# Optimization experiments

Hardware: AMD Instinct MI355X
Metric: run time of the kernel (lower is better)

The kernel has to match this reference:

```python
import jax, jax.numpy as jnp
import numpy as np

EPS = 1.1920929e-07  # torch float32 eps used by nn.RMSNorm(elementwise_affine=False)
MAX_LR = 0.01        # default_step_transform_max_lr


def rmsnorm(x):
    return x * jax.lax.rsqrt(jnp.mean(jnp.square(x), axis=-1, keepdims=True) + EPS)


def assoc_scan(gates, inputs):
    # first-order recurrence x_t = gates_t * x_{t-1} + inputs_t along axis=1
    gates = jnp.broadcast_to(gates, inputs.shape)

    def combine(a, b):
        ag, ax = a
        bg, bx = b
        return (ag * bg, bg * ax + bx)

    _, out = jax.lax.associative_scan(combine, (gates, inputs), axis=1)
    return out


def setup_inputs():
    key = jax.random.key(0)
    ks = jax.random.split(key, 12)
    b, t, dim, heads, d, c = 4, 8192, 512, 8, 64, 64
    di = heads * d
    sc_dim = dim ** -0.5
    sc_d = d ** -0.5
    return {
        'seq': jax.random.normal(ks[0], (b, t, dim), jnp.float32),
        'w1': jax.random.normal(ks[1], (d, d), jnp.float32) * sc_d,
        'w2': jax.random.normal(ks[2], (d, d), jnp.float32) * sc_d,
        'Wq': jax.random.normal(ks[3], (dim, di), jnp.float32) * sc_dim,
        'Wkv': jax.random.normal(ks[4], (dim, 2 * di), jnp.float32) * sc_dim,
        'Wstep': jax.random.normal(ks[5], (dim, heads), jnp.float32) * sc_dim,
        'Wmom': jax.random.normal(ks[6], (dim, heads), jnp.float32) * sc_dim,
        'Wdecay': jax.random.normal(ks[7], (dim, heads), jnp.float32) * sc_dim,
        'Wgate': jax.random.normal(ks[8], (dim, heads), jnp.float32) * sc_dim,
        'Wcombine': jax.random.normal(ks[9], (di, dim), jnp.float32) * (di ** -0.5),
        'gamma': jnp.zeros((heads, 1, d), jnp.float32),
        'chunk_size': 64,
    }


def _forward(seq, w1, w2, Wq, Wkv, Wstep, Wmom, Wdecay, Wgate, Wcombine, gamma, c):
    b, t, dim = seq.shape
    heads = Wstep.shape[1]
    d = w1.shape[0]
    n = t // c          # number of chunks (seq_len assumed multiple of chunk_size)
    bh = b * heads

    # ---------------- store_memories ----------------
    s = rmsnorm(seq)  # store_norm
    # adaptive per-token lr: sigmoid * max_lr, per head -> (bh, n, c)
    lr = jax.nn.sigmoid(jnp.einsum('btd,dh->bth', s, Wstep)) * MAX_LR
    lr = lr.transpose(0, 2, 1).reshape(bh, n, c)
    # per-chunk momentum / decay gates from chunk-mean of seq
    s_chunk = s.reshape(b, n, c, dim).mean(axis=2)
    mom_gate = jax.nn.sigmoid(jnp.einsum('bnd,dh->bnh', s_chunk, Wmom)).transpose(0, 2, 1).reshape(bh, n, 1)
    decay = jax.nn.sigmoid(jnp.einsum('bnd,dh->bnh', s_chunk, Wdecay)).transpose(0, 2, 1).reshape(bh, n, 1)
    # keys / values, split heads, chunked -> (bh, n, c, d)
    kv = jnp.einsum('btd,de->bte', s, Wkv)
    k, v = jnp.split(kv, 2, axis=-1)
    split = lambda x: x.reshape(b, t, heads, d).transpose(0, 2, 1, 3).reshape(bh, n, c, d)
    k, v = split(k), split(v)

    def chunk_loss(ws, kc, lrc, vc):
        x = kc @ ws[0]
        x = jax.nn.silu(x) @ ws[1]
        return jnp.sum(jnp.mean(jnp.square(x - vc), axis=-1) * lrc)

    # per-sample (per bh, per chunk) grads of the tiny MLP
    grad_fn = jax.grad(chunk_loss, argnums=0)
    g1, g2 = jax.vmap(jax.vmap(grad_fn, in_axes=(None, 0, 0, 0)), in_axes=(None, 0, 0, 0))((w1, w2), k, lr, v)

    updates = []
    for g in (g1, g2):
        flat = (-g).reshape(bh, n, d * d)        # surprises
        momentum = assoc_scan(mom_gate, flat)     # momentum recurrence
        upd = assoc_scan(1.0 - decay, momentum)   # decayed weight-update recurrence
        updates.append(upd.reshape(bh, n, d, d))

    # ---------------- retrieve_memories ----------------
    r = rmsnorm(seq)[:, c - 1:]                   # retrieve_norm + causal shift
    pad = (-r.shape[1]) % c                       # pad to multiple of chunk_size (= c-1 here)
    r = jnp.pad(r, ((0, 0), (0, pad), (0, 0)))    # (b, n*c, dim)
    q = jnp.einsum('btd,de->bte', r, Wq)
    qs = q.reshape(b, n * c, heads, d).transpose(0, 2, 1, 3).reshape(bh, n, c, d)
    # apply per-chunk fast weights (base + update)
    x = jnp.einsum('bncd,bnde->bnce', qs, w1 + updates[0])
    x = jax.nn.silu(x)
    x = jnp.einsum('bncd,bnde->bnce', x, w2 + updates[1])
    vals = x.reshape(b, heads, n * c, d)
    vals = rmsnorm(vals) * (gamma + 1.0)          # MultiheadRMSNorm (gamma zeros-init)
    gate = jax.nn.sigmoid(jnp.einsum('btd,dh->bth', r, Wgate))  # retrieve_gate
    vals = vals * gate.transpose(0, 2, 1)[..., None]
    out = vals.transpose(0, 2, 1, 3).reshape(b, n * c, heads * d)  # merge heads
    out = jnp.einsum('bte,ed->btd', out, Wcombine)                 # combine_heads
    out = jnp.pad(out, ((0, 0), (c - 1, 0), (0, 0)))[:, :t]       # shift back, crop
    return out


def reference(seq, w1, w2, Wq, Wkv, Wstep, Wmom, Wdecay, Wgate, Wcombine, gamma, chunk_size):
    return _forward(seq, w1, w2, Wq, Wkv, Wstep, Wmom, Wdecay, Wgate, Wcombine, gamma, chunk_size)
```

## Files before the change

kernel.cpp:

```cpp
#include <hip/hip_runtime.h>
#include <cstdint>

#define EPS     1.1920929e-07f
#define MAX_LR  0.01f
#define BB      4
#define TT      8192
#define DIMM    512
#define HH      8
#define DD      64
#define CC      64
#define NN      128
#define BHH     32
#define LDSP    72

typedef __attribute__((ext_vector_type(8))) short short8;
typedef __attribute__((ext_vector_type(4))) float f32x4;

__device__ __forceinline__ float sigmoidf_(float x){ return 1.0f/(1.0f+__expf(-x)); }
__device__ __forceinline__ float bf2f(uint32_t lo16){ return __uint_as_float(lo16<<16); }
__device__ __forceinline__ uint16_t f2bf(float f){
    uint32_t x = __float_as_uint(f);
    return (uint16_t)((x + 0x7fffu + ((x>>16)&1u)) >> 16);
}
__device__ __forceinline__ uint32_t pk2(float a, float b){
    return (uint32_t)f2bf(a) | ((uint32_t)f2bf(b)<<16);
}
__device__ __forceinline__ void gload_lds16(const uint16_t* g, uint16_t* l){
    __builtin_amdgcn_global_load_lds(
        (const __attribute__((address_space(1))) unsigned int*)g,
        (__attribute__((address_space(3))) unsigned int*)l, 16, 0, 0);
}

__device__ __forceinline__ void gemm64(const uint16_t* A, const uint16_t* B,
                                       int strip, int q, int col, f32x4* acc)
{
    #pragma unroll
    for (int ks=0; ks<64; ks+=32){
        short8 af = *(const short8*)&A[(strip*16+col)*LDSP + ks + q*8];
        #pragma unroll
        for (int nt=0;nt<4;nt++){
            short8 bf = *(const short8*)&B[(nt*16+col)*LDSP + ks + q*8];
            acc[nt] = __builtin_amdgcn_mfma_f32_16x16x32_bf16(af, bf, acc[nt], 0,0,0);
        }
    }
}

__device__ __forceinline__ void gemm64g(const uint16_t* __restrict__ Ag,
                                        const uint16_t* B,
                                        int strip, int q, int col, f32x4* acc)
{
    #pragma unroll
    for (int ks=0; ks<64; ks+=32){
        short8 af = *(const short8*)&Ag[(strip*16+col)*DD + ks + q*8];
        #pragma unroll
        for (int nt=0;nt<4;nt++){
            short8 bf = *(const short8*)&B[(nt*16+col)*LDSP + ks + q*8];
            acc[nt] = __builtin_amdgcn_mfma_f32_16x16x32_bf16(af, bf, acc[nt], 0,0,0);
        }
    }
}

__global__ __launch_bounds__(256) void k_prep(
    const float* __restrict__ Wkv, const float* __restrict__ Wq,
    const float* __restrict__ Wcomb, const float* __restrict__ Wstep,
    const float* __restrict__ Wgate, const float* __restrict__ w1,
    const float* __restrict__ w2,
    uint16_t* __restrict__ btkv, uint16_t* __restrict__ btq,
    uint16_t* __restrict__ btc, uint16_t* __restrict__ wsg,
    uint16_t* __restrict__ w1t_bf, uint16_t* __restrict__ w2t_bf,
    uint16_t* __restrict__ w2b_bf, float* __restrict__ w1t_f,
    float* __restrict__ w2t_f)
{
    __shared__ float tile[32][33];
    __shared__ float t1[64][65];
    __shared__ float t2[64][65];
    int blk = blockIdx.x;
    if (blk < 1024){
        const float* in; uint16_t* out; int Ncols; int i;
        if (blk < 512){ in=Wkv; out=btkv; Ncols=1024; i=blk; }
        else if (blk < 768){ in=Wq; out=btq; Ncols=512; i=blk-512; }
        else { in=Wcomb; out=btc; Ncols=512; i=blk-768; }
        int nx = Ncols>>5;
        int bx = (i % nx)*32, by = (i / nx)*32;
        int lx = threadIdx.x&31, ly = threadIdx.x>>5;
        #pragma unroll
        for (int r=0;r<4;r++)
            tile[ly+8*r][lx] = in[(size_t)(by+ly+8*r)*Ncols + bx+lx];
        __syncthreads();
        #pragma unroll
        for (int r=0;r<4;r++)
            out[(size_t)(bx+ly+8*r)*DIMM + by+lx] = f2bf(tile[lx][ly+8*r]);
    } else if (blk < 1056){
        int g = (blk-1024)*256 + threadIdx.x;
        int j = g >> 9, k = g & 511;
        float v = (j < HH) ? Wstep[k*HH + j] : Wgate[k*HH + (j-HH)];
        wsg[j*DIMM + k] = f2bf(v);
    } else {
        int tx = threadIdx.x & 63, ty = threadIdx.x >> 6;
        #pragma unroll
        for (int i=0;i<16;i++){
            int row = ty*16 + i;
            float v1 = w1[row*DD + tx];
            float v2 = w2[row*DD + tx];
            t1[row][tx] = v1;
            t2[row][tx] = v2;
            w2b_bf[row*DD + tx] = f2bf(v2);
        }
        __syncthreads();
        #pragma unroll
        for (int i=0;i<16;i++){
            int row = ty*16 + i;
            float v1 = t1[tx][row];
            float v2 = t2[tx][row];
            w1t_f[row*DD + tx] = v1;
            w1t_bf[row*DD + tx] = f2bf(v1);
            w2t_f[row*DD + tx] = v2;
            w2t_bf[row*DD + tx] = f2bf(v2);
        }
    }
}

__global__ __launch_bounds__(256) void k_scale(
    const float* __restrict__ seq, float* __restrict__ scale,
    uint16_t* __restrict__ sbf)
{
    int wave = threadIdx.x >> 6, lane = threadIdx.x & 63;
    int row = blockIdx.x*4 + wave;
    const float4* sp = (const float4*)&seq[(size_t)row*DIMM + lane*8];
    float4 x0 = sp[0], x1 = sp[1];
    float ss = x0.x*x0.x + x0.y*x0.y + x0.z*x0.z + x0.w*x0.w
             + x1.x*x1.x + x1.y*x1.y + x1.z*x1.z + x1.w*x1.w;
    #pragma unroll
    for (int o=32;o;o>>=1) ss += __shfl_xor(ss,o,64);
    float sc = rsqrtf(ss*(1.0f/DIMM)+EPS);
    if (lane==0) scale[row] = sc;
    uint4 v;
    v.x = pk2(x0.x*sc, x0.y*sc);
    v.y = pk2(x0.z*sc, x0.w*sc);
    v.z = pk2(x1.x*sc, x1.y*sc);
    v.w = pk2(x1.z*sc, x1.w*sc);
    *(uint4*)&sbf[(size_t)row*DIMM + lane*8] = v;
}

__global__ __launch_bounds__(256) void k_lr_gate(
    const uint16_t* __restrict__ sbf, const uint16_t* __restrict__ wsg,
    float* __restrict__ lr_t, float* __restrict__ gate_t)
{
    __shared__ uint16_t Asl[128][LDSP];
    int tid = threadIdx.x;
    int w = tid>>6, lane = tid&63, q = lane>>4, col = lane&15;
    int m0 = blockIdx.x*128;

    f32x4 acc[2];
    acc[0] = (f32x4){0.f,0.f,0.f,0.f};
    acc[1] = (f32x4){0.f,0.f,0.f,0.f};

    for (int k0=0;k0<DIMM;k0+=64){
        #pragma unroll
        for (int s=0;s<4;s++){
            int seg = s*256 + tid;
            int row = seg>>3, kk = seg&7;
            uint4 v = *(const uint4*)&sbf[(size_t)(m0+row)*DIMM + k0 + kk*8];
            *(uint4*)&Asl[row][kk*8] = v;
        }
        __syncthreads();
        #pragma unroll
        for (int ks=0;ks<64;ks+=32){
            short8 bf = *(const short8*)&wsg[(size_t)col*DIMM + k0 + ks + q*8];
            #pragma unroll
            for (int mt=0;mt<2;mt++){
                short8 af = *(const short8*)&Asl[w*32 + mt*16 + col][ks + q*8];
                acc[mt] = __builtin_amdgcn_mfma_f32_16x16x32_bf16(af, bf, acc[mt], 0,0,0);
            }
        }
        __syncthreads();
    }

    #pragma unroll
    for (int mt=0;mt<2;mt++){
        #pragma unroll
        for (int reg=0;reg<4;reg++){
            int m = m0 + w*32 + mt*16 + q*4 + reg;
            int b = m>>13, t = m&8191;
            float val = sigmoidf_(acc[mt][reg]);
            if (col < HH){
                lr_t[(size_t)m*HH + col] = val*MAX_LR;
            } else {
                int j = t-63;
                if (j >= 0)
                    gate_t[((size_t)b*TT + j)*HH + (col-HH)] = val;
            }
        }
    }
}

__global__ __launch_bounds__(512) void k_chunk_gates(
    const uint16_t* __restrict__ sbf,
    const float* __restrict__ Wmom, const float* __restrict__ Wdecay,
    float* __restrict__ mom, float* __restrict__ dec)
{
    int blk = blockIdx.x;
    int b = blk>>7, n = blk&127;
    int tid = threadIdx.x;
    size_t base = ((size_t)b*TT + n*CC)*DIMM + tid;
    float acc=0.f;
    #pragma unroll 8
    for (int j=0;j<CC;j++) acc += bf2f(sbf[base + (size_t)j*DIMM]);
    __shared__ float sm[DIMM];
    sm[tid] = acc*(1.0f/CC);
    __syncthreads();
    int wid = tid>>6, lane = tid&63;
    float d1=0.f, d2=0.f;
    #pragma unroll
    for (int i=0;i<8;i++){
        int idx=i*64+lane; float sv=sm[idx];
        d1 += sv*Wmom[idx*HH+wid];
        d2 += sv*Wdecay[idx*HH+wid];
    }
    #pragma unroll
    for (int o=32;o;o>>=1){ d1+=__shfl_down(d1,o,64); d2+=__shfl_down(d2,o,64); }
    if (lane==0){
        mom[(b*HH+wid)*NN + n] = sigmoidf_(d1);
        dec[(b*HH+wid)*NN + n] = sigmoidf_(d2);
    }
}

template<int MODE>
__global__ __launch_bounds__(256) void k_gemm_mfma(
    const void* __restrict__ Av, const uint16_t* __restrict__ Bt,
    const float* __restrict__ scale, void* __restrict__ out0,
    void* __restrict__ out1)
{
    __shared__ __align__(16) uint16_t shmem[128*72 + 128*64];
    uint16_t* Asl = shmem;
    uint16_t* Bsl = shmem + 128*72;
    __shared__ float sscale[128];
    int tid = threadIdx.x;
    int wave = tid>>6, lane = tid&63;
    int q = lane>>4, col = lane&15;
    int bid = blockIdx.y*gridDim.x + blockIdx.x;
    int xcd = bid & 7, local = bid >> 3;
    int mper = gridDim.y >> 3;
    int m0 = (xcd*mper + local/gridDim.x)*128;
    int n0 = (local%gridDim.x)*128;
    int m_off = (wave&1)*64, n_off = (wave>>1)*64;

    if (MODE==1){
        if (tid<128) sscale[tid] = scale[m0+tid];
        __syncthreads();
    }

    f32x4 acc[4][4];
    #pragma unroll
    for (int i=0;i<4;i++)
        #pragma unroll
        for (int j=0;j<4;j++) acc[i][j] = (f32x4){0.f,0.f,0.f,0.f};

    int srow = wave*32 + (lane>>3);
    int sgs  = lane&7;

    for (int k0=0;k0<DIMM;k0+=64){
        if (MODE!=1){
            const uint16_t* A = (const uint16_t*)Av;
            #pragma unroll
            for (int s=0;s<4;s++){
                int r = srow + s*8;
                gload_lds16(&A[(size_t)(m0+r)*DIMM + k0 + ((sgs ^ (r&7))<<3)],
                            &Asl[(wave*32 + s*8)*64]);
            }
        } else {
            const float* A = (const float*)Av;
            #pragma unroll
            for (int s=0;s<4;s++){
                int seg = s*256 + tid;
                int row = seg>>3, kk = seg&7;
                float sc = sscale[row];
                const float4* ap = (const float4*)&A[(size_t)(m0+row)*DIMM + k0 + kk*8];
                float4 a0 = ap[0], a1 = ap[1];
                uint4 v;
                v.x = pk2(a0.x*sc, a0.y*sc);
                v.y = pk2(a0.z*sc, a0.w*sc);
                v.z = pk2(a1.x*sc, a1.y*sc);
                v.w = pk2(a1.z*sc, a1.w*sc);
                *(uint4*)&Asl[row*72 + kk*8] = v;
            }
        }
        #pragma unroll
        for (int s=0;s<4;s++){
            int r = srow + s*8;
            gload_lds16(&Bt[(size_t)(n0+r)*DIMM + k0 + ((sgs ^ (r&7))<<3)],
                        &Bsl[(wave*32 + s*8)*64]);
        }
        __syncthreads();
        #pragma unroll
        for (int ks=0;ks<64;ks+=32){
            short8 af[4], bf[4];
            int g = q + (ks>>3);
            #pragma unroll
            for (int mt=0;mt<4;mt++){
                int r = m_off + mt*16 + col;
                if (MODE==1)
                    af[mt] = *(const short8*)&Asl[r*72 + ks + q*8];
                else
                    af[mt] = *(const short8*)&Asl[r*64 + ((g ^ (r&7))<<3)];
            }
            #pragma unroll
            for (int nt=0;nt<4;nt++){
                int rb = n_off + nt*16 + col;
                bf[nt] = *(const short8*)&Bsl[rb*64 + ((g ^ (rb&7))<<3)];
            }
            #pragma unroll
            for (int mt=0;mt<4;mt++)
                #pragma unroll
                for (int nt=0;nt<4;nt++)
                    acc[mt][nt] = __builtin_amdgcn_mfma_f32_16x16x32_bf16(
                        af[mt], bf[nt], acc[mt][nt], 0, 0, 0);
        }
        __syncthreads();
    }

    if (MODE==0){
        #pragma unroll
        for (int mt=0;mt<4;mt++)
            #pragma unroll
            for (int reg=0;reg<4;reg++){
                int lrow = m_off + mt*16 + q*4 + reg;
                #pragma unroll
                for (int nt=0;nt<4;nt++){
                    int le = n_off + nt*16 + col;
                    shmem[lrow*128 + le] = f2bf(acc[mt][nt][reg]);
                }
            }
        __syncthreads();
        uint16_t* basep = (uint16_t*)((n0 < 512) ? out0 : out1);
        int h0 = (n0 & 511) >> 6;
        #pragma unroll
        for (int p=0;p<8;p++){
            int idx = p*256 + tid;
            int lrow = idx >> 4, seg = idx & 15;
            int m = m0 + lrow;
            int b = m>>13, t = m&8191;
            int h = h0 + (seg>>3);
            int dk = (seg&7)*8;
            uint4 v = *(const uint4*)&shmem[lrow*128 + seg*8];
            *(uint4*)&basep[((size_t)(b*HH+h)*TT + t)*DD + dk] = v;
        }
    } else {
        #pragma unroll
        for (int mt=0;mt<4;mt++){
            #pragma unroll
            for (int reg=0;reg<4;reg++){
                int m = m0 + m_off + mt*16 + q*4 + reg;
                int b = m>>13, t = m&8191;
                if (MODE==1){
                    int j = t-63;
                    if (j>=0){
                        #pragma unroll
                        for (int nt=0;nt<4;nt++){
                            int e = n0 + n_off + nt*16 + col;
                            int h = e>>6, dk = e&63;
                            ((uint16_t*)out0)[((size_t)(b*HH+h)*TT + j)*DD + dk] = f2bf(acc[mt][nt][reg]);
                        }
                    }
                } else {
                    int tp = t + 63;
                    if (tp < TT){
                        #pragma unroll
                        for (int nt=0;nt<4;nt++){
                            int e = n0 + n_off + nt*16 + col;
                            ((float*)out0)[((size_t)b*TT + tp)*DIMM + e] = acc[mt][nt][reg];
                        }
                    }
                }
            }
        }
    }
}

__global__ __launch_bounds__(256) void k_grad(
    const uint16_t* __restrict__ kbuf, const uint16_t* __restrict__ vbuf,
    const float* __restrict__ lr_t, const uint16_t* __restrict__ w1t_bf,
    const uint16_t* __restrict__ w2t_bf, const uint16_t* __restrict__ w2b_bf,
    uint16_t* __restrict__ g1T, uint16_t* __restrict__ g2T)
{
    __shared__ uint16_t lds[5*64*LDSP];
    __shared__ float lr_sh[64];
    uint16_t* kcB  = lds + 0*64*LDSP;
    uint16_t* kcT  = lds + 1*64*LDSP;
    uint16_t* vB   = lds + 2*64*LDSP;
    uint16_t* hA   = lds + 3*64*LDSP;
    uint16_t* hB   = lds + 4*64*LDSP;
    uint16_t* dxA  = kcB;
    uint16_t* dxB  = vB;
    uint16_t* dx1T = hB;

    int bhn = blockIdx.x;
    int bh = bhn>>7, n = bhn&127;
    int b = bh>>3, h = bh&7;
    int tid = threadIdx.x, tx = tid&15, ty = tid>>4;
    int w = tid>>6, lane = tid&63, q = lane>>4, col = lane&15;
    size_t cbase = ((size_t)bh*TT + n*CC)*DD;

    #pragma unroll
    for (int r=0;r<4;r++){
        int row = ty*4+r;
        ushort4 k4 = *(const ushort4*)&kbuf[cbase + row*DD + tx*4];
        *(ushort4*)&kcB[row*LDSP + tx*4] = k4;
        kcT[(tx*4+0)*LDSP + row] = k4.x;
        kcT[(tx*4+1)*LDSP + row] = k4.y;
        kcT[(tx*4+2)*LDSP + row] = k4.z;
        kcT[(tx*4+3)*LDSP + row] = k4.w;
        ushort4 v4 = *(const ushort4*)&vbuf[cbase + row*DD + tx*4];
        *(ushort4*)&vB[row*LDSP + tx*4] = v4;
    }
    if (tid < 64) lr_sh[tid] = lr_t[((size_t)b*TT + n*CC + tid)*HH + h];
    __syncthreads();

    f32x4 a1[4];
    #pragma unroll
    for (int i=0;i<4;i++) a1[i]=(f32x4){0.f,0.f,0.f,0.f};
    gemm64g(w1t_bf, kcB, w, q, col, a1);
    float sg[16], hr[16];
    #pragma unroll
    for (int nt=0;nt<4;nt++)
        #pragma unroll
        for (int reg=0;reg<4;reg++){
            int idx = nt*4+reg;
            float x = a1[nt][reg];
            float sgm = sigmoidf_(x);
            sg[idx]=sgm; hr[idx]=x*sgm;
            int d1 = w*16 + q*4 + reg;
            int token = nt*16 + col;
            uint16_t hv = f2bf(x*sgm);
            hA[d1*LDSP + token] = hv;
            hB[token*LDSP + d1] = hv;
        }
    __syncthreads();

    f32x4 a2[4];
    #pragma unroll
    for (int i=0;i<4;i++) a2[i]=(f32x4){0.f,0.f,0.f,0.f};
    gemm64g(w2t_bf, hB, w, q, col, a2);
    __syncthreads();
    #pragma unroll
    for (int nt=0;nt<4;nt++)
        #pragma unroll
        for (int reg=0;reg<4;reg++){
            int d2 = w*16 + q*4 + reg;
            int token = nt*16 + col;
            float vv = bf2f(vB[token*LDSP + d2]);
            float dx = (2.0f/DD)*lr_sh[token]*(a2[nt][reg]-vv);
            uint16_t dv = f2bf(dx);
            dxA[d2*LDSP + token] = dv;
            dxB[token*LDSP + d2] = dv;
        }
    __syncthreads();

    f32x4 a3[4];
    #pragma unroll
    for (int i=0;i<4;i++) a3[i]=(f32x4){0.f,0.f,0.f,0.f};
    gemm64(dxA, hA, w, q, col, a3);
    f32x4 a4[4];
    #pragma unroll
    for (int i=0;i<4;i++) a4[i]=(f32x4){0.f,0.f,0.f,0.f};
    gemm64g(w2b_bf, dxB, w, q, col, a4);

    size_t gb = (size_t)bhn*4096;
    #pragma unroll
    for (int nt=0;nt<4;nt++)
        #pragma unroll
        for (int reg=0;reg<4;reg++){
            int d2 = w*16 + q*4 + reg;
            int d1 = nt*16 + col;
            g2T[gb + d2*DD + d1] = f2bf(-a3[nt][reg]);
        }
    #pragma unroll
    for (int nt=0;nt<4;nt++)
        #pragma unroll
        for (int reg=0;reg<4;reg++){
            int idx = nt*4+reg;
            int d1 = w*16 + q*4 + reg;
            int token = nt*16 + col;
            float dsl = sg[idx] + hr[idx]*(1.f-sg[idx]);
            dx1T[d1*LDSP + token] = f2bf(a4[nt][reg]*dsl);
        }
    __syncthreads();

    f32x4 a5[4];
    #pragma unroll
    for (int i=0;i<4;i++) a5[i]=(f32x4){0.f,0.f,0.f,0.f};
    gemm64(dx1T, kcT, w, q, col, a5);
    #pragma unroll
    for (int nt=0;nt<4;nt++)
        #pragma unroll
        for (int reg=0;reg<4;reg++){
            int d1 = w*16 + q*4 + reg;
            int p  = nt*16 + col;
            g1T[gb + d1*DD + p] = f2bf(-a5[nt][reg]);
        }
}

__global__ __launch_bounds__(256) void k_scan(
    uint16_t* __restrict__ g1, uint16_t* __restrict__ g2,
    const float* __restrict__ mom, const float* __restrict__ dec)
{
    int blk = blockIdx.x;
    int arr = blk>>7; int rem = blk&127;
    int bh = rem>>2; int eg = rem&3;
    int e4 = eg*1024 + threadIdx.x*4;
    uint16_t* gp = arr ? g2 : g1;
    __shared__ float smg[NN], sdc[NN];
    if (threadIdx.x < NN){
        smg[threadIdx.x] = mom[bh*NN+threadIdx.x];
        sdc[threadIdx.x] = 1.f - dec[bh*NN+threadIdx.x];
    }
    __syncthreads();
    size_t base = (size_t)bh*NN*4096 + e4;
    float m0=0.f,m1=0.f,m2=0.f,m3=0.f, u0=0.f,u1=0.f,u2=0.f,u3=0.f;
    uint2 p0 = *(const uint2*)&gp[base];
    uint2 p1 = *(const uint2*)&gp[base + 4096];
    uint2 p2 = *(const uint2*)&gp[base + 2*4096];
    uint2 p3 = *(const uint2*)&gp[base + 3*4096];
    for (int t=0; t<NN; t+=4){
        uint2 c0=p0, c1=p1, c2=p2, c3=p3;
        if (t+4 < NN){
            p0 = *(const uint2*)&gp[base + (size_t)(t+4)*4096];
            p1 = *(const uint2*)&gp[base + (size_t)(t+5)*4096];
            p2 = *(const uint2*)&gp[base + (size_t)(t+6)*4096];
            p3 = *(const uint2*)&gp[base + (size_t)(t+7)*4096];
        }
        #pragma unroll
        for (int j=0;j<4;j++){
            uint2 c = (j==0)?c0:(j==1)?c1:(j==2)?c2:c3;
            float g = smg[t+j], d = sdc[t+j];
            float v0 = bf2f(c.x&0xffffu), v1 = bf2f(c.x>>16);
            float v2 = bf2f(c.y&0xffffu), v3 = bf2f(c.y>>16);
            m0 = fmaf(g,m0,v0); u0 = fmaf(d,u0,m0);
            m1 = fmaf(g,m1,v1); u1 = fmaf(d,u1,m1);
            m2 = fmaf(g,m2,v2); u2 = fmaf(d,u2,m2);
            m3 = fmaf(g,m3,v3); u3 = fmaf(d,u3,m3);
            uint2 r; r.x = pk2(u0,u1); r.y = pk2(u2,u3);
            *(uint2*)&gp[base + (size_t)(t+j)*4096] = r;
        }
    }
}

__global__ __launch_bounds__(256) void k_retrieve(
    const uint16_t* __restrict__ qbuf, const uint16_t* __restrict__ u1T,
    const uint16_t* __restrict__ u2T, const float* __restrict__ w1Tf,
    const float* __restrict__ w2Tf, const float* __restrict__ gamma,
    const float* __restrict__ gate_t, uint16_t* __restrict__ y)
{
    __shared__ uint16_t qc[64*LDSP];
    __shared__ uint16_t W1s[64*LDSP];
    __shared__ uint16_t W2s[64*LDSP];
    __shared__ uint16_t hB[64*LDSP];
    __shared__ float gate_sh[64], gam_sh[64];
    int bhn = blockIdx.x;
    int bh = bhn>>7, n = bhn&127;
    int b = bh>>3, h = bh&7;
    int tid = threadIdx.x, tx = tid&15, ty = tid>>4;
    int w = tid>>6, lane = tid&63, q = lane>>4, col = lane&15;
    size_t cbase = ((size_t)bh*TT + n*CC)*DD;
    size_t ub = (size_t)bhn*4096;

    #pragma unroll
    for (int r=0;r<4;r++){
        int row = ty*4+r;
        *(ushort4*)&qc[row*LDSP + tx*4] =
            *(const ushort4*)&qbuf[cbase + row*DD + tx*4];
        ushort4 u14 = *(const ushort4*)&u1T[ub + row*DD + tx*4];
        float4 w1v = *(const float4*)&w1Tf[row*DD + tx*4];
        ushort4 s1;
        s1.x = f2bf(w1v.x + bf2f(u14.x));
        s1.y = f2bf(w1v.y + bf2f(u14.y));
        s1.z = f2bf(w1v.z + bf2f(u14.z));
        s1.w = f2bf(w1v.w + bf2f(u14.w));
        *(ushort4*)&W1s[row*LDSP + tx*4] = s1;
        ushort4 u24 = *(const ushort4*)&u2T[ub + row*DD + tx*4];
        float4 w2v = *(const float4*)&w2Tf[row*DD + tx*4];
        ushort4 s2;
        s2.x = f2bf(w2v.x + bf2f(u24.x));
        s2.y = f2bf(w2v.y + bf2f(u24.y));
        s2.z = f2bf(w2v.z + bf2f(u24.z));
        s2.w = f2bf(w2v.w + bf2f(u24.w));
        *(ushort4*)&W2s[row*LDSP + tx*4] = s2;
    }
    if (tid < 64){
        gate_sh[tid] = gate_t[((size_t)b*TT + n*CC + tid)*HH + h];
        gam_sh[tid]  = gamma[h*DD + tid];
    }
    __syncthreads();

    f32x4 a1[4];
    #pragma unroll
    for (int i=0;i<4;i++) a1[i]=(f32x4){0.f,0.f,0.f,0.f};
    gemm64(qc, W1s, w, q, col, a1);
    #pragma unroll
    for (int nt=0;nt<4;nt++)
        #pragma unroll
        for (int reg=0;reg<4;reg++){
            float x = a1[nt][reg];
            int token = w*16 + q*4 + reg;
            int d1 = nt*16 + col;
            hB[token*LDSP + d1] = f2bf(x*sigmoidf_(x));
        }
    __syncthreads();

    f32x4 a2[4];
    #pragma unroll
    for (int i=0;i<4;i++) a2[i]=(f32x4){0.f,0.f,0.f,0.f};
    gemm64(hB, W2s, w, q, col, a2);
    #pragma unroll
    for (int reg=0;reg<4;reg++){
        float p = 0.f;
        #pragma unroll
        for (int nt=0;nt<4;nt++) p += a2[nt][reg]*a2[nt][reg];
        p += __shfl_xor(p,1,64);
        p += __shfl_xor(p,2,64);
        p += __shfl_xor(p,4,64);
        p += __shfl_xor(p,8,64);
        float sclv = rsqrtf(p*(1.0f/DD)+EPS);
        int token = w*16 + q*4 + reg;
        float gt = gate_sh[token];
        size_t yb = ((size_t)b*TT + n*CC + token)*DIMM + h*DD;
        #pragma unroll
        for (int nt=0;nt<4;nt++){
            int d2 = nt*16 + col;
            y[yb + d2] = f2bf(a2[nt][reg]*sclv*(1.f+gam_sh[d2])*gt);
        }
    }
}

__global__ __launch_bounds__(256) void k_zero(
    uint16_t* __restrict__ qbuf, float* __restrict__ out, float* __restrict__ gate_t)
{
    int g = blockIdx.x*256 + threadIdx.x;
    const int QN = BHH*63*DD;
    const int ON = BB*63*DIMM;
    const int GN = BB*63*HH;
    if (g < QN){
        int bh = g/4032; int r = g - bh*4032;
        int j = 8129 + (r>>6); int dk = r&63;
        qbuf[((size_t)bh*TT + j)*DD + dk] = 0;
    } else if (g < QN+ON){
        int g2i = g - QN;
        int b = g2i/(63*512); int r = g2i - b*63*512;
        int t = r>>9; int e = r&511;
        out[((size_t)b*TT + t)*DIMM + e] = 0.f;
    } else if (g < QN+ON+GN){
        int g3 = g - QN - ON;
        int b = g3/(63*HH); int r = g3 - b*63*HH;
        int j = 8129 + (r>>3); int hh = r&7;
        gate_t[((size_t)b*TT + j)*HH + hh] = 0.f;
    }
}

extern "C" void kernel_launch(void* const* d_in, const int* in_sizes, int n_in,
                              void* d_out, int out_size, void* d_ws, size_t ws_size,
                              hipStream_t stream)
{
    (void)in_sizes; (void)n_in; (void)out_size; (void)ws_size;
    const float* seq    = (const float*)d_in[0];
    const float* w1     = (const float*)d_in[1];
    const float* w2     = (const float*)d_in[2];
    const float* Wq     = (const float*)d_in[3];
    const float* Wkv    = (const float*)d_in[4];
    const float* Wstep  = (const float*)d_in[5];
    const float* Wmom   = (const float*)d_in[6];
    const float* Wdecay = (const float*)d_in[7];
    const float* Wgate  = (const float*)d_in[8];
    const float* Wcomb  = (const float*)d_in[9];
    const float* gamma  = (const float*)d_in[10];
    float* out = (float*)d_out;

    float* scale = (float*)d_ws;
    float* lr_t  = scale + 32768;
    float* gate_t= lr_t + 262144;
    float* mom   = gate_t + 262144;
    float* dec   = mom + 4096;
    float* w1t_f = dec + 4096;
    float* w2t_f = w1t_f + 4096;
    uint16_t* w1t_bf = (uint16_t*)(w2t_f + 4096);
    uint16_t* w2t_bf = w1t_bf + 4096;
    uint16_t* w2b_bf = w2t_bf + 4096;
    uint16_t* btkv = w2b_bf + 4096;
    uint16_t* btq  = btkv + 1024*512;
    uint16_t* btc  = btq  + 512*512;
    uint16_t* kb = btc + 512*512;
    uint16_t* vb = kb + 16777216;
    uint16_t* g1 = vb + 16777216;
    uint16_t* g2 = g1 + 16777216;
    uint16_t* sbf = g1;
    uint16_t* wsg = g2;

    k_prep <<<1057, 256, 0, stream>>>(Wkv, Wq, Wcomb, Wstep, Wgate, w1, w2,
                                      btkv, btq, btc, wsg,
                                      w1t_bf, w2t_bf, w2b_bf, w1t_f, w2t_f);
    k_scale     <<<8192, 256, 0, stream>>>(seq, scale, sbf);
    k_lr_gate   <<<256, 256, 0, stream>>>(sbf, wsg, lr_t, gate_t);
    k_chunk_gates<<<BB*NN, 512, 0, stream>>>(sbf, Wmom, Wdecay, mom, dec);
    k_gemm_mfma<0><<<dim3(8, 256), 256, 0, stream>>>(sbf, btkv, nullptr, kb, vb);
    k_grad   <<<BHH*NN, 256, 0, stream>>>(kb, vb, lr_t, w1t_bf, w2t_bf, w2b_bf, g1, g2);
    k_scan   <<<256, 256, 0, stream>>>(g1, g2, mom, dec);
    k_gemm_mfma<1><<<dim3(4, 256), 256, 0, stream>>>(seq, btq, scale, kb , nullptr);
    k_zero   <<<1017, 256, 0, stream>>>(kb , out, gate_t);
    k_retrieve<<<BHH*NN, 256, 0, stream>>>(kb , g1, g2, w1t_f, w2t_f, gamma, gate_t, vb );
    k_gemm_mfma<2><<<dim3(4, 256), 256, 0, stream>>>(vb , btc, nullptr, out, nullptr);
}
```

Before: 357.7 us.

## Fuse small kernels and use swizzled LDS with direct global-to-LDS loads in grad

Merges the lr/gate projection and the chunk momentum/decay gates into one launch. It also folds the padding zero-fill into the scan kernel, so two launches go away and the small kernels can overlap. In k_grad, the k/v chunk loads now use global_load_lds into an XOR-swizzled 64-wide LDS layout, and the transpose is built from LDS instead of scalar scattered stores. A templated gemm helper handles the padded and swizzled operand layouts. The zero-fill now runs before the Q projection rather than after, which relies on that GEMM never writing the padded rows.

```diff
diff --git a/kernel.cpp b/kernel.cpp
--- a/kernel.cpp
+++ b/kernel.cpp
@@ -31,30 +31,24 @@
         (__attribute__((address_space(3))) unsigned int*)l, 16, 0, 0);
 }
 
-__device__ __forceinline__ void gemm64(const uint16_t* A, const uint16_t* B,
-                                       int strip, int q, int col, f32x4* acc)
+template<int AM, int BM>
+__device__ __forceinline__ void gemm64u(const uint16_t* A, const uint16_t* B,
+                                        int strip, int q, int col, f32x4* acc)
 {
     #pragma unroll
     for (int ks=0; ks<64; ks+=32){
-        short8 af = *(const short8*)&A[(strip*16+col)*LDSP + ks + q*8];
+        int g = q + (ks>>3);
+        int ra = strip*16+col;
+        short8 af;
+        if (AM==0)      af = *(const short8*)&A[ra*LDSP + ks + q*8];
+        else if (AM==1) af = *(const short8*)&A[ra*64 + ((g ^ (ra&7))<<3)];
+        else            af = *(const short8*)&A[ra*DD + ks + q*8];
         #pragma unroll
         for (int nt=0;nt<4;nt++){
-            short8 bf = *(const short8*)&B[(nt*16+col)*LDSP + ks + q*8];
-            acc[nt] = __builtin_amdgcn_mfma_f32_16x16x32_bf16(af, bf, acc[nt], 0,0,0);
-        }
-    }
-}
-
-__device__ __forceinline__ void gemm64g(const uint16_t* __restrict__ Ag,
-                                        const uint16_t* B,
-                                        int strip, int q, int col, f32x4* acc)
-{
-    #pragma unroll
-    for (int ks=0; ks<64; ks+=32){
-        short8 af = *(const short8*)&Ag[(strip*16+col)*DD + ks + q*8];
-        #pragma unroll
-        for (int nt=0;nt<4;nt++){
-            short8 bf = *(const short8*)&B[(nt*16+col)*LDSP + ks + q*8];
+            int rb = nt*16+col;
+            short8 bf;
+            if (BM==0) bf = *(const short8*)&B[rb*LDSP + ks + q*8];
+            else       bf = *(const short8*)&B[rb*64 + ((g ^ (rb&7))<<3)];
             acc[nt] = __builtin_amdgcn_mfma_f32_16x16x32_bf16(af, bf, acc[nt], 0,0,0);
         }
     }
@@ -142,86 +136,92 @@
     *(uint4*)&sbf[(size_t)row*DIMM + lane*8] = v;
 }
 
-__global__ __launch_bounds__(256) void k_lr_gate(
+__global__ __launch_bounds__(256) void k_post_sbf(
     const uint16_t* __restrict__ sbf, const uint16_t* __restrict__ wsg,
-    float* __restrict__ lr_t, float* __restrict__ gate_t)
+    const float* __restrict__ Wmom, const float* __restrict__ Wdecay,
+    float* __restrict__ lr_t, float* __restrict__ gate_t,
+    float* __restrict__ mom, float* __restrict__ dec)
 {
     __shared__ uint16_t Asl[128][LDSP];
+    __shared__ float sm[DIMM];
+    int blk = blockIdx.x;
     int tid = threadIdx.x;
-    int w = tid>>6, lane = tid&63, q = lane>>4, col = lane&15;
-    int m0 = blockIdx.x*128;
-
-    f32x4 acc[2];
-    acc[0] = (f32x4){0.f,0.f,0.f,0.f};
-    acc[1] = (f32x4){0.f,0.f,0.f,0.f};
-
-    for (int k0=0;k0<DIMM;k0+=64){
-        #pragma unroll
-        for (int s=0;s<4;s++){
-            int seg = s*256 + tid;
-            int row = seg>>3, kk = seg&7;
-            uint4 v = *(const uint4*)&sbf[(size_t)(m0+row)*DIMM + k0 + kk*8];
-            *(uint4*)&Asl[row][kk*8] = v;
-        }
+    if (blk < 256){
+        int w = tid>>6, lane = tid&63, q = lane>>4, col = lane&15;
+        int m0 = blk*128;
+        f32x4 acc[2];
+        acc[0] = (f32x4){0.f,0.f,0.f,0.f};
+        acc[1] = (f32x4){0.f,0.f,0.f,0.f};
+        for (int k0=0;k0<DIMM;k0+=64){
+            #pragma unroll
+            for (int s=0;s<4;s++){
+                int seg = s*256 + tid;
+                int row = seg>>3, kk = seg&7;
+                uint4 v = *(const uint4*)&sbf[(size_t)(m0+row)*DIMM + k0 + kk*8];
+                *(uint4*)&Asl[row][kk*8] = v;
+            }
+            __syncthreads();
+            #pragma unroll
+            for (int ks=0;ks<64;ks+=32){
+                short8 bf = *(const short8*)&wsg[(size_t)col*DIMM + k0 + ks + q*8];
+                #pragma unroll
+                for (int mt=0;mt<2;mt++){
+                    short8 af = *(const short8*)&Asl[w*32 + mt*16 + col][ks + q*8];
+                    acc[mt] = __builtin_amdgcn_mfma_f32_16x16x32_bf16(af, bf, acc[mt], 0,0,0);
+                }
+            }
+            __syncthreads();
+        }
+        #pragma unroll
+        for (int mt=0;mt<2;mt++){
+            #pragma unroll
+            for (int reg=0;reg<4;reg++){
+                int m = m0 + w*32 + mt*16 + q*4 + reg;
+                int b = m>>13, t = m&8191;
+                float val = sigmoidf_(acc[mt][reg]);
+                if (col < HH){
+                    lr_t[(size_t)m*HH + col] = val*MAX_LR;
+                } else {
+                    int j = t-63;
+                    if (j >= 0)
+                        gate_t[((size_t)b*TT + j)*HH + (col-HH)] = val;
+                }
+            }
+        }
+    } else {
+        int cblk = blk - 256;
+        int b = cblk>>7, n = cblk&127;
+        size_t base = ((size_t)b*TT + n*CC)*DIMM + tid;
+        float a0=0.f, a1=0.f;
+        #pragma unroll 8
+        for (int j=0;j<CC;j++){
+            a0 += bf2f(sbf[base + (size_t)j*DIMM]);
+            a1 += bf2f(sbf[base + 256 + (size_t)j*DIMM]);
+        }
+        sm[tid] = a0*(1.0f/CC);
+        sm[tid+256] = a1*(1.0f/CC);
         __syncthreads();
-        #pragma unroll
-        for (int ks=0;ks<64;ks+=32){
-            short8 bf = *(const short8*)&wsg[(size_t)col*DIMM + k0 + ks + q*8];
-            #pragma unroll
-            for (int mt=0;mt<2;mt++){
-                short8 af = *(const short8*)&Asl[w*32 + mt*16 + col][ks + q*8];
-                acc[mt] = __builtin_amdgcn_mfma_f32_16x16x32_bf16(af, bf, acc[mt], 0,0,0);
-            }
-        }
-        __syncthreads();
-    }
-
-    #pragma unroll
-    for (int mt=0;mt<2;mt++){
-        #pragma unroll
-        for (int reg=0;reg<4;reg++){
-            int m = m0 + w*32 + mt*16 + q*4 + reg;
-            int b = m>>13, t = m&8191;
-            float val = sigmoidf_(acc[mt][reg]);
-            if (col < HH){
-                lr_t[(size_t)m*HH + col] = val*MAX_LR;
-            } else {
-                int j = t-63;
-                if (j >= 0)
-                    gate_t[((size_t)b*TT + j)*HH + (col-HH)] = val;
-            }
-        }
-    }
-}
-
-__global__ __launch_bounds__(512) void k_chunk_gates(
-    const uint16_t* __restrict__ sbf,
-    const float* __restrict__ Wmom, const float* __restrict__ Wdecay,
-    float* __restrict__ mom, float* __restrict__ dec)
-{
-    int blk = blockIdx.x;
-    int b = blk>>7, n = blk&127;
-    int tid = threadIdx.x;
-    size_t base = ((size_t)b*TT + n*CC)*DIMM + tid;
-    float acc=0.f;
-    #pragma unroll 8
-    for (int j=0;j<CC;j++) acc += bf2f(sbf[base + (size_t)j*DIMM]);
-    __shared__ float sm[DIMM];
-    sm[tid] = acc*(1.0f/CC);
-    __syncthreads();
-    int wid = tid>>6, lane = tid&63;
-    float d1=0.f, d2=0.f;
-    #pragma unroll
-    for (int i=0;i<8;i++){
-        int idx=i*64+lane; float sv=sm[idx];
-        d1 += sv*Wmom[idx*HH+wid];
-        d2 += sv*Wdecay[idx*HH+wid];
-    }
-    #pragma unroll
-    for (int o=32;o;o>>=1){ d1+=__shfl_down(d1,o,64); d2+=__shfl_down(d2,o,64); }
-    if (lane==0){
-        mom[(b*HH+wid)*NN + n] = sigmoidf_(d1);
-        dec[(b*HH+wid)*NN + n] = sigmoidf_(d2);
+        int wid = tid>>6, lane = tid&63;
+        float d1a=0.f, d1b=0.f, d2a=0.f, d2b=0.f;
+        #pragma unroll
+        for (int i=0;i<8;i++){
+            int idx=i*64+lane; float sv=sm[idx];
+            d1a += sv*Wmom[idx*HH+wid];
+            d1b += sv*Wmom[idx*HH+wid+4];
+            d2a += sv*Wdecay[idx*HH+wid];
+            d2b += sv*Wdecay[idx*HH+wid+4];
+        }
+        #pragma unroll
+        for (int o=32;o;o>>=1){
+            d1a+=__shfl_down(d1a,o,64); d1b+=__shfl_down(d1b,o,64);
+            d2a+=__shfl_down(d2a,o,64); d2b+=__shfl_down(d2b,o,64);
+        }
+        if (lane==0){
+            mom[(b*HH+wid)*NN + n]   = sigmoidf_(d1a);
+            mom[(b*HH+wid+4)*NN + n] = sigmoidf_(d1b);
+            dec[(b*HH+wid)*NN + n]   = sigmoidf_(d2a);
+            dec[(b*HH+wid+4)*NN + n] = sigmoidf_(d2b);
+        }
     }
 }
 
@@ -383,13 +383,12 @@
     const uint16_t* __restrict__ w2t_bf, const uint16_t* __restrict__ w2b_bf,
     uint16_t* __restrict__ g1T, uint16_t* __restrict__ g2T)
 {
-    __shared__ uint16_t lds[5*64*LDSP];
+    __shared__ __align__(16) uint16_t kcB[64*64];
+    __shared__ __align__(16) uint16_t kcT[64*64];
+    __shared__ __align__(16) uint16_t vB [64*64];
+    __shared__ uint16_t hA[64*LDSP];
+    __shared__ uint16_t hB[64*LDSP];
     __shared__ float lr_sh[64];
-    uint16_t* kcB  = lds + 0*64*LDSP;
-    uint16_t* kcT  = lds + 1*64*LDSP;
-    uint16_t* vB   = lds + 2*64*LDSP;
-    uint16_t* hA   = lds + 3*64*LDSP;
-    uint16_t* hB   = lds + 4*64*LDSP;
     uint16_t* dxA  = kcB;
     uint16_t* dxB  = vB;
     uint16_t* dx1T = hB;
@@ -397,29 +396,48 @@
     int bhn = blockIdx.x;
     int bh = bhn>>7, n = bhn&127;
     int b = bh>>3, h = bh&7;
-    int tid = threadIdx.x, tx = tid&15, ty = tid>>4;
+    int tid = threadIdx.x;
     int w = tid>>6, lane = tid&63, q = lane>>4, col = lane&15;
     size_t cbase = ((size_t)bh*TT + n*CC)*DD;
 
-    #pragma unroll
-    for (int r=0;r<4;r++){
-        int row = ty*4+r;
-        ushort4 k4 = *(const ushort4*)&kbuf[cbase + row*DD + tx*4];
-        *(ushort4*)&kcB[row*LDSP + tx*4] = k4;
-        kcT[(tx*4+0)*LDSP + row] = k4.x;
-        kcT[(tx*4+1)*LDSP + row] = k4.y;
-        kcT[(tx*4+2)*LDSP + row] = k4.z;
-        kcT[(tx*4+3)*LDSP + row] = k4.w;
-        ushort4 v4 = *(const ushort4*)&vbuf[cbase + row*DD + tx*4];
-        *(ushort4*)&vB[row*LDSP + tx*4] = v4;
+    int srow8 = lane>>3, sgs = lane&7;
+    #pragma unroll
+    for (int s=0;s<2;s++){
+        int r = w*16 + s*8 + srow8;
+        gload_lds16(&kbuf[cbase + (size_t)r*DD + ((sgs ^ (r&7))<<3)],
+                    &kcB[(w*16 + s*8)*64]);
+        gload_lds16(&vbuf[cbase + (size_t)r*DD + ((sgs ^ (r&7))<<3)],
+                    &vB[(w*16 + s*8)*64]);
     }
     if (tid < 64) lr_sh[tid] = lr_t[((size_t)b*TT + n*CC + tid)*HH + h];
     __syncthreads();
 
+    #pragma unroll
+    for (int it=0; it<2; it++){
+        int task = tid + it*256;
+        int p = task & 63, g = task >> 6;
+        ushort4 lo, hi;
+        uint16_t* dst;
+        {
+            int pg = p>>3, pw = p&7;
+            lo.x = kcB[(g*8+0)*64 + ((pg ^ 0)<<3) + pw];
+            lo.y = kcB[(g*8+1)*64 + ((pg ^ 1)<<3) + pw];
+            lo.z = kcB[(g*8+2)*64 + ((pg ^ 2)<<3) + pw];
+            lo.w = kcB[(g*8+3)*64 + ((pg ^ 3)<<3) + pw];
+            hi.x = kcB[(g*8+4)*64 + ((pg ^ 4)<<3) + pw];
+            hi.y = kcB[(g*8+5)*64 + ((pg ^ 5)<<3) + pw];
+            hi.z = kcB[(g*8+6)*64 + ((pg ^ 6)<<3) + pw];
+            hi.w = kcB[(g*8+7)*64 + ((pg ^ 7)<<3) + pw];
+            dst = &kcT[p*64 + ((g ^ (p&7))<<3)];
+        }
+        *(ushort4*)dst = lo;
+        *(ushort4*)(dst+4) = hi;
+    }
+
     f32x4 a1[4];
     #pragma unroll
     for (int i=0;i<4;i++) a1[i]=(f32x4){0.f,0.f,0.f,0.f};
-    gemm64g(w1t_bf, kcB, w, q, col, a1);
+    gemm64u<2,1>(w1t_bf, kcB, w, q, col, a1);
     float sg[16], hr[16];
     #pragma unroll
     for (int nt=0;nt<4;nt++)
@@ -440,7 +458,7 @@
     f32x4 a2[4];
     #pragma unroll
     for (int i=0;i<4;i++) a2[i]=(f32x4){0.f,0.f,0.f,0.f};
-    gemm64g(w2t_bf, hB, w, q, col, a2);
+    gemm64u<2,0>(w2t_bf, hB, w, q, col, a2);
     __syncthreads();
     #pragma unroll
     for (int nt=0;nt<4;nt++)
@@ -448,22 +466,23 @@
         for (int reg=0;reg<4;reg++){
             int d2 = w*16 + q*4 + reg;
             int token = nt*16 + col;
-            float vv = bf2f(vB[token*LDSP + d2]);
+            int vaddr = token*64 + (((d2>>3) ^ (token&7))<<3) + (d2&7);
+            float vv = bf2f(vB[vaddr]);
             float dx = (2.0f/DD)*lr_sh[token]*(a2[nt][reg]-vv);
             uint16_t dv = f2bf(dx);
-            dxA[d2*LDSP + token] = dv;
-            dxB[token*LDSP + d2] = dv;
+            dxA[d2*64 + (((token>>3) ^ (d2&7))<<3) + (token&7)] = dv;
+            dxB[vaddr] = dv;
         }
     __syncthreads();
 
     f32x4 a3[4];
     #pragma unroll
     for (int i=0;i<4;i++) a3[i]=(f32x4){0.f,0.f,0.f,0.f};
-    gemm64(dxA, hA, w, q, col, a3);
+    gemm64u<1,0>(dxA, hA, w, q, col, a3);
     f32x4 a4[4];
     #pragma unroll
     for (int i=0;i<4;i++) a4[i]=(f32x4){0.f,0.f,0.f,0.f};
-    gemm64g(w2b_bf, dxB, w, q, col, a4);
+    gemm64u<2,1>(w2b_bf, dxB, w, q, col, a4);
 
     size_t gb = (size_t)bhn*4096;
     #pragma unroll
@@ -489,7 +508,7 @@
     f32x4 a5[4];
     #pragma unroll
     for (int i=0;i<4;i++) a5[i]=(f32x4){0.f,0.f,0.f,0.f};
-    gemm64(dx1T, kcT, w, q, col, a5);
+    gemm64u<0,1>(dx1T, kcT, w, q, col, a5);
     #pragma unroll
     for (int nt=0;nt<4;nt++)
         #pragma unroll
@@ -500,47 +519,71 @@
         }
 }
 
-__global__ __launch_bounds__(256) void k_scan(
+__global__ __launch_bounds__(256) void k_scan_zero(
     uint16_t* __restrict__ g1, uint16_t* __restrict__ g2,
-    const float* __restrict__ mom, const float* __restrict__ dec)
+    const float* __restrict__ mom, const float* __restrict__ dec,
+    uint16_t* __restrict__ qbuf, float* __restrict__ out,
+    float* __restrict__ gate_t)
 {
     int blk = blockIdx.x;
-    int arr = blk>>7; int rem = blk&127;
-    int bh = rem>>2; int eg = rem&3;
-    int e4 = eg*1024 + threadIdx.x*4;
-    uint16_t* gp = arr ? g2 : g1;
-    __shared__ float smg[NN], sdc[NN];
-    if (threadIdx.x < NN){
-        smg[threadIdx.x] = mom[bh*NN+threadIdx.x];
-        sdc[threadIdx.x] = 1.f - dec[bh*NN+threadIdx.x];
-    }
-    __syncthreads();
-    size_t base = (size_t)bh*NN*4096 + e4;
-    float m0=0.f,m1=0.f,m2=0.f,m3=0.f, u0=0.f,u1=0.f,u2=0.f,u3=0.f;
-    uint2 p0 = *(const uint2*)&gp[base];
-    uint2 p1 = *(const uint2*)&gp[base + 4096];
-    uint2 p2 = *(const uint2*)&gp[base + 2*4096];
-    uint2 p3 = *(const uint2*)&gp[base + 3*4096];
-    for (int t=0; t<NN; t+=4){
-        uint2 c0=p0, c1=p1, c2=p2, c3=p3;
-        if (t+4 < NN){
-            p0 = *(const uint2*)&gp[base + (size_t)(t+4)*4096];
-            p1 = *(const uint2*)&gp[base + (size_t)(t+5)*4096];
-            p2 = *(const uint2*)&gp[base + (size_t)(t+6)*4096];
-            p3 = *(const uint2*)&gp[base + (size_t)(t+7)*4096];
-        }
-        #pragma unroll
-        for (int j=0;j<4;j++){
-            uint2 c = (j==0)?c0:(j==1)?c1:(j==2)?c2:c3;
-            float g = smg[t+j], d = sdc[t+j];
-            float v0 = bf2f(c.x&0xffffu), v1 = bf2f(c.x>>16);
-            float v2 = bf2f(c.y&0xffffu), v3 = bf2f(c.y>>16);
-            m0 = fmaf(g,m0,v0); u0 = fmaf(d,u0,m0);
-            m1 = fmaf(g,m1,v1); u1 = fmaf(d,u1,m1);
-            m2 = fmaf(g,m2,v2); u2 = fmaf(d,u2,m2);
-            m3 = fmaf(g,m3,v3); u3 = fmaf(d,u3,m3);
-            uint2 r; r.x = pk2(u0,u1); r.y = pk2(u2,u3);
-            *(uint2*)&gp[base + (size_t)(t+j)*4096] = r;
+    if (blk < 256){
+        int arr = blk>>7; int rem = blk&127;
+        int bh = rem>>2; int eg = rem&3;
+        int e4 = eg*1024 + threadIdx.x*4;
+        uint16_t* gp = arr ? g2 : g1;
+        __shared__ float smg[NN], sdc[NN];
+        if (threadIdx.x < NN){
+            smg[threadIdx.x] = mom[bh*NN+threadIdx.x];
+            sdc[threadIdx.x] = 1.f - dec[bh*NN+threadIdx.x];
+        }
+        __syncthreads();
+        size_t base = (size_t)bh*NN*4096 + e4;
+        float m0=0.f,m1=0.f,m2=0.f,m3=0.f, u0=0.f,u1=0.f,u2=0.f,u3=0.f;
+        uint2 p0 = *(const uint2*)&gp[base];
+        uint2 p1 = *(const uint2*)&gp[base + 4096];
+        uint2 p2 = *(const uint2*)&gp[base + 2*4096];
+        uint2 p3 = *(const uint2*)&gp[base + 3*4096];
+        for (int t=0; t<NN; t+=4){
+            uint2 c0=p0, c1=p1, c2=p2, c3=p3;
+            if (t+4 < NN){
+                p0 = *(const uint2*)&gp[base + (size_t)(t+4)*4096];
+                p1 = *(const uint2*)&gp[base + (size_t)(t+5)*4096];
+                p2 = *(const uint2*)&gp[base + (size_t)(t+6)*4096];
+                p3 = *(const uint2*)&gp[base + (size_t)(t+7)*4096];
+            }
+            #pragma unroll
+            for (int j=0;j<4;j++){
+                uint2 c = (j==0)?c0:(j==1)?c1:(j==2)?c2:c3;
+                float g = smg[t+j], d = sdc[t+j];
+                float v0 = bf2f(c.x&0xffffu), v1 = bf2f(c.x>>16);
+                float v2 = bf2f(c.y&0xffffu), v3 = bf2f(c.y>>16);
+                m0 = fmaf(g,m0,v0); u0 = fmaf(d,u0,m0);
+                m1 = fmaf(g,m1,v1); u1 = fmaf(d,u1,m1);
+                m2 = fmaf(g,m2,v2); u2 = fmaf(d,u2,m2);
+                m3 = fmaf(g,m3,v3); u3 = fmaf(d,u3,m3);
+                uint2 r; r.x = pk2(u0,u1); r.y = pk2(u2,u3);
+                *(uint2*)&gp[base + (size_t)(t+j)*4096] = r;
+            }
+        }
+    } else {
+        int g = (blk-256)*256 + threadIdx.x;
+        const int QN = BHH*63*DD;
+        const int ON = BB*63*DIMM;
+        const int GN = BB*63*HH;
+        if (g < QN){
+            int bh = g/4032; int r = g - bh*4032;
+            int j = 8129 + (r>>6); int dk = r&63;
+            qbuf[((size_t)bh*TT + j)*DD + dk] = 0;
+        } else if (g < QN+ON){
+            int g2i = g - QN;
+            int b = g2i/(63*512); int r = g2i - b*63*512;
+            int t = r>>9; int e = r&511;
+            out[((size_t)b*TT + t)*DIMM + e] = 0.f;
+        } else if (g < QN+ON+GN){
+            int g3 = g - QN - ON;
+            int b = g3/(63*HH); int r = g3 - b*63*HH;
+            int j = 8129 + (r>>3); int hh = r&7;
+            gate_t[((size_t)b*TT + j)*HH + hh] = 0.f;
         }
     }
 }
@@ -595,7 +638,7 @@
     f32x4 a1[4];
     #pragma unroll
     for (int i=0;i<4;i++) a1[i]=(f32x4){0.f,0.f,0.f,0.f};
-    gemm64(qc, W1s, w, q, col, a1);
+    gemm64u<0,0>(qc, W1s, w, q, col, a1);
     #pragma unroll
     for (int nt=0;nt<4;nt++)
         #pragma unroll
@@ -610,7 +653,7 @@
     f32x4 a2[4];
     #pragma unroll
     for (int i=0;i<4;i++) a2[i]=(f32x4){0.f,0.f,0.f,0.f};
-    gemm64(hB, W2s, w, q, col, a2);
+    gemm64u<0,0>(hB, W2s, w, q, col, a2);
     #pragma unroll
     for (int reg=0;reg<4;reg++){
         float p = 0.f;
@@ -629,30 +672,6 @@
             int d2 = nt*16 + col;
             y[yb + d2] = f2bf(a2[nt][reg]*sclv*(1.f+gam_sh[d2])*gt);
         }
-    }
-}
-
-__global__ __launch_bounds__(256) void k_zero(
-    uint16_t* __restrict__ qbuf, float* __restrict__ out, float* __restrict__ gate_t)
-{
-    int g = blockIdx.x*256 + threadIdx.x;
-    const int QN = BHH*63*DD;
-    const int ON = BB*63*DIMM;
-    const int GN = BB*63*HH;
-    if (g < QN){
-        int bh = g/4032; int r = g - bh*4032;
-        int j = 8129 + (r>>6); int dk = r&63;
-        qbuf[((size_t)bh*TT + j)*DD + dk] = 0;
-    } else if (g < QN+ON){
-        int g2i = g - QN;
-        int b = g2i/(63*512); int r = g2i - b*63*512;
-        int t = r>>9; int e = r&511;
-        out[((size_t)b*TT + t)*DIMM + e] = 0.f;
-    } else if (g < QN+ON+GN){
-        int g3 = g - QN - ON;
-        int b = g3/(63*HH); int r = g3 - b*63*HH;
-        int j = 8129 + (r>>3); int hh = r&7;
-        gate_t[((size_t)b*TT + j)*HH + hh] = 0.f;
     }
 }
 
@@ -697,14 +716,13 @@
     k_prep <<<1057, 256, 0, stream>>>(Wkv, Wq, Wcomb, Wstep, Wgate, w1, w2,
                                       btkv, btq, btc, wsg,
                                       w1t_bf, w2t_bf, w2b_bf, w1t_f, w2t_f);
-    k_scale     <<<8192, 256, 0, stream>>>(seq, scale, sbf);
-    k_lr_gate   <<<256, 256, 0, stream>>>(sbf, wsg, lr_t, gate_t);
-    k_chunk_gates<<<BB*NN, 512, 0, stream>>>(sbf, Wmom, Wdecay, mom, dec);
+    k_scale    <<<8192, 256, 0, stream>>>(seq, scale, sbf);
+    k_post_sbf <<<768, 256, 0, stream>>>(sbf, wsg, Wmom, Wdecay,
+                                         lr_t, gate_t, mom, dec);
     k_gemm_mfma<0><<<dim3(8, 256), 256, 0, stream>>>(sbf, btkv, nullptr, kb, vb);
     k_grad   <<<BHH*NN, 256, 0, stream>>>(kb, vb, lr_t, w1t_bf, w2t_bf, w2b_bf, g1, g2);
-    k_scan   <<<256, 256, 0, stream>>>(g1, g2, mom, dec);
+    k_scan_zero<<<1273, 256, 0, stream>>>(g1, g2, mom, dec, kb , out, gate_t);
     k_gemm_mfma<1><<<dim3(4, 256), 256, 0, stream>>>(seq, btq, scale, kb , nullptr);
-    k_zero   <<<1017, 256, 0, stream>>>(kb , out, gate_t);
     k_retrieve<<<BHH*NN, 256, 0, stream>>>(kb , g1, g2, w1t_f, w2t_f, gamma, gate_t, vb );
     k_gemm_mfma<2><<<dim3(4, 256), 256, 0, stream>>>(vb , btc, nullptr, out, nullptr);
 }
```

Result: faster. 342.9 us (-4.1%).
